# Performance work log

Hardware: AMD Instinct MI355X
Metric: run time of the kernel (lower is better)

## Reference

```python
import jax, jax.numpy as jnp
import numpy as np

HIDDEN = 1024
HEADS = 16
HEAD_DIM = HIDDEN // HEADS
BATCH = 2
SEQ = 2048


def setup_inputs() -> dict:
    key = jax.random.key(0)
    k1, k2, k3 = jax.random.split(key, 3)
    hidden_states = jax.random.normal(k1, (BATCH, SEQ, HIDDEN), dtype=jnp.float32)
    # torch Linear(hidden, 3*hidden) applies x @ W.T; we store the transposed
    # weight directly so the math is x @ W_qkv. Scale ~ fan_in init.
    W_qkv = jax.random.normal(k2, (HIDDEN, 3 * HIDDEN), dtype=jnp.float32) / np.sqrt(HIDDEN)
    W_o = jax.random.normal(k3, (HIDDEN, HIDDEN), dtype=jnp.float32) / np.sqrt(HIDDEN)
    return {"hidden_states": hidden_states, "W_qkv": W_qkv, "W_o": W_o}


def reference(hidden_states, W_qkv, W_o):
    B, S, _ = hidden_states.shape
    scale = 1.0 / np.sqrt(HEAD_DIM)
    qkv = hidden_states @ W_qkv                       # [B, S, 3*H*D]
    qkv = qkv.reshape(B, S, 3, HEADS, HEAD_DIM)
    qkv = jnp.transpose(qkv, (2, 0, 3, 1, 4))         # [3, B, H, S, D]
    q, k, v = qkv[0], qkv[1], qkv[2]
    # The chunked online-softmax path computes exactly softmax(qk^T*scale)v.
    scores = jnp.einsum("bhsd,bhtd->bhst", q, k) * scale  # [B, H, S, S]
    probs = jax.nn.softmax(scores, axis=-1)
    out = jnp.einsum("bhst,bhtd->bhsd", probs, v)     # [B, H, S, D]
    out = jnp.transpose(out, (0, 2, 1, 3)).reshape(B, S, HIDDEN)
    return out @ W_o
```

## Files before the change

kernel.cpp:

```cpp
#include <hip/hip_runtime.h>
#include <hip/hip_bf16.h>
#include <cstdint>

typedef __bf16 bf16_t;
typedef __bf16 bf16x8 __attribute__((ext_vector_type(8)));
typedef __bf16 bf16x4 __attribute__((ext_vector_type(4)));
typedef __bf16 bf16x2 __attribute__((ext_vector_type(2)));
typedef float  f32x4  __attribute__((ext_vector_type(4)));
typedef float  f32x16 __attribute__((ext_vector_type(16)));
typedef unsigned uint4v __attribute__((ext_vector_type(4)));

#define AS1 __attribute__((address_space(1)))
#define AS3 __attribute__((address_space(3)))

static __device__ __forceinline__ void gld_lds16(const void* g, void* l) {
  __builtin_amdgcn_global_load_lds((AS1 void*)g, (AS3 void*)l, 16, 0, 0);
}

static __device__ __forceinline__ unsigned pk2t(float a, float b) {
  return __builtin_amdgcn_perm(__builtin_bit_cast(unsigned, a),
                               __builtin_bit_cast(unsigned, b), 0x03020706u);
}

__global__ __launch_bounds__(256) void prep_k(const float* __restrict__ x,
                                              bf16_t* __restrict__ xb,
                                              const float* __restrict__ wqkv,
                                              bf16_t* __restrict__ wqkvT,
                                              const float* __restrict__ wo,
                                              bf16_t* __restrict__ woT) {
  int bid = blockIdx.x;
  if (bid < 4096) {
    const int i = bid * 256 + threadIdx.x;
    float4 v = ((const float4*)x)[i];
    bf16x4 o;
    o[0] = (bf16_t)v.x; o[1] = (bf16_t)v.y; o[2] = (bf16_t)v.z; o[3] = (bf16_t)v.w;
    *(bf16x4*)(xb + (size_t)i * 4) = o;
    return;
  }
  __shared__ float tile[32][33];
  const float* in; bf16_t* out; int N, bx, by;
  if (bid < 7168) { bid -= 4096; in = wqkv; out = wqkvT; N = 3072; bx = bid % 96; by = bid / 96; }
  else            { bid -= 7168; in = wo;   out = woT;   N = 1024; bx = bid & 31; by = bid >> 5; }
  const int t = threadIdx.x, c = t & 31, r0 = t >> 5;
#pragma unroll
  for (int i = 0; i < 4; ++i) {
    int r = r0 + i * 8;
    tile[r][c] = in[(size_t)(by * 32 + r) * N + bx * 32 + c];
  }
  __syncthreads();
#pragma unroll
  for (int i = 0; i < 4; ++i) {
    int r = r0 + i * 8;
    out[(size_t)(bx * 32 + r) * 1024 + by * 32 + c] = (bf16_t)tile[c][r];
  }
}

template <int KDIM>
static __device__ __forceinline__ void gemm128_pipe(const bf16_t* __restrict__ A,
                                                    const bf16_t* __restrict__ Bt,
                                                    char* lds, f32x4 acc[4][4],
                                                    int bm, int bn) {
  constexpr int NK = KDIM / 32;
  const int t = threadIdx.x;
  const int lr = t & 15, g = (t >> 4) & 3;
  const int w = t >> 6, wr = w >> 1, wc = w & 1;

  auto bufA = [&](int i) { return lds + (i % 3) * 8192; };
  auto bufB = [&](int i) { return lds + 24576 + (i % 3) * 8192; };

  auto stage = [&](int i) {
    const int kt = i * 32;
    char* la = bufA(i);
    char* lb = bufB(i);
#pragma unroll
    for (int c = 0; c < 2; ++c) {
      const int idx = c * 256 + t;
      const int row = idx >> 2, cb = idx & 3;
      const int off = ((t & 192) + c * 256) * 16;
      gld_lds16(A  + (size_t)(bm * 128 + row) * KDIM + kt + cb * 8, la + off);
      gld_lds16(Bt + (size_t)(bn * 128 + row) * KDIM + kt + cb * 8, lb + off);
    }
  };

  stage(0);
  stage(1);
  asm volatile("s_waitcnt vmcnt(4)" ::: "memory");
  __builtin_amdgcn_sched_barrier(0);
  __builtin_amdgcn_s_barrier();

  for (int j = 0; j < NK; ++j) {
    if (j + 2 < NK) {
      stage(j + 2);
      asm volatile("s_waitcnt vmcnt(8)" ::: "memory");
    } else if (j + 1 < NK) {
      asm volatile("s_waitcnt vmcnt(4)" ::: "memory");
    } else {
      asm volatile("s_waitcnt vmcnt(0)" ::: "memory");
    }
    __builtin_amdgcn_sched_barrier(0);
    __builtin_amdgcn_s_barrier();
    const char* laR = bufA(j);
    const char* lbR = bufB(j);
    bf16x8 af[4], bv[4];
#pragma unroll
    for (int mi = 0; mi < 4; ++mi)
      af[mi] = *(const bf16x8*)(laR + (wr * 64 + mi * 16 + lr) * 64 + g * 16);
#pragma unroll
    for (int ni = 0; ni < 4; ++ni)
      bv[ni] = *(const bf16x8*)(lbR + (wc * 64 + ni * 16 + lr) * 64 + g * 16);
    __builtin_amdgcn_s_setprio(1);
#pragma unroll
    for (int mi = 0; mi < 4; ++mi)
#pragma unroll
      for (int ni = 0; ni < 4; ++ni)
        acc[mi][ni] = __builtin_amdgcn_mfma_f32_16x16x32_bf16(af[mi], bv[ni], acc[mi][ni], 0, 0, 0);
    __builtin_amdgcn_s_setprio(0);
    __builtin_amdgcn_sched_barrier(0);
    __builtin_amdgcn_s_barrier();
  }
}

__global__ __launch_bounds__(256) void gemm_qkv_k(const bf16_t* __restrict__ xb,
                                                  const bf16_t* __restrict__ wt,
                                                  bf16_t* __restrict__ Qo,
                                                  bf16_t* __restrict__ Ko,
                                                  bf16_t* __restrict__ Vto) {
  __shared__ __align__(16) char lds[49152];
  const int bm = blockIdx.x, bn = blockIdx.y;
  f32x4 acc[4][4] = {};
  gemm128_pipe<1024>(xb, wt, lds, acc, bm, bn);
  const float cs = 0.18033688011112042f;
  const int t = threadIdx.x, lr = t & 15, g = (t >> 4) & 3, w = t >> 6, wr = w >> 1, wc = w & 1;
  const int row0 = bm * 128 + wr * 64, col0 = bn * 128 + wc * 64;
#pragma unroll
  for (int mi = 0; mi < 4; ++mi) {
    const int row = row0 + mi * 16 + g * 4;
    const int b = row >> 11, s = row & 2047;
#pragma unroll
    for (int ni = 0; ni < 4; ++ni) {
      const int col = col0 + ni * 16 + lr;
      const int t3 = col >> 10, rem = col & 1023, h = rem >> 6, d = rem & 63;
      const int bh = b * 16 + h;
#pragma unroll
      for (int r = 0; r < 4; ++r) {
        const float av = acc[mi][ni][r];
        if (t3 == 0)      Qo[((size_t)bh * 2048 + s + r) * 64 + d] = (bf16_t)(av * cs);
        else if (t3 == 1) Ko[((size_t)bh * 2048 + s + r) * 64 + d] = (bf16_t)av;
        else {
          const int kv = s + r;
          const int q3 = (kv >> 2) & 7;
          const int dq = (q3 & 4) | ((q3 & 1) << 1) | ((q3 >> 1) & 1);
          const int kvp = (kv & ~31) | (dq << 2) | (kv & 3);
          Vto[((size_t)bh * 64 + d) * 2048 + kvp] = (bf16_t)av;
        }
      }
    }
  }
}

__global__ __launch_bounds__(256) void gemm_o_k(const bf16_t* __restrict__ attn,
                                                const bf16_t* __restrict__ wot,
                                                float* __restrict__ out) {
  __shared__ __align__(16) char lds[49152];
  const int bm = blockIdx.x, bn = blockIdx.y;
  f32x4 acc[4][4] = {};
  gemm128_pipe<1024>(attn, wot, lds, acc, bm, bn);
  const int t = threadIdx.x, lr = t & 15, g = (t >> 4) & 3, w = t >> 6, wr = w >> 1, wc = w & 1;
  const int row0 = bm * 128 + wr * 64, col0 = bn * 128 + wc * 64;
#pragma unroll
  for (int mi = 0; mi < 4; ++mi) {
    const int row = row0 + mi * 16 + g * 4;
#pragma unroll
    for (int ni = 0; ni < 4; ++ni) {
      const int col = col0 + ni * 16 + lr;
#pragma unroll
      for (int r = 0; r < 4; ++r)
        out[(size_t)(row + r) * 1024 + col] = acc[mi][ni][r];
    }
  }
}

__global__ __launch_bounds__(256, 2) void attn_k(const bf16_t* __restrict__ Q,
                                                 const bf16_t* __restrict__ K,
                                                 const bf16_t* __restrict__ Vt,
                                                 bf16_t* __restrict__ Ao) {
  __shared__ __align__(16) char smem[32768];
  const int t = threadIdx.x, w = t >> 6, l = t & 63;
  const int ql = l & 31, hi = l >> 5;
  const int orig = blockIdx.y * 16 + blockIdx.x;
  const int swz = (orig & 7) * 64 + (orig >> 3);
  const int qblk = swz & 15, bh = swz >> 4;
  const int b = bh >> 4, h = bh & 15;
  const bf16_t* Qb = Q  + (size_t)bh * 2048 * 64;
  const bf16_t* Kb = K  + (size_t)bh * 2048 * 64;
  const bf16_t* Vb = Vt + (size_t)bh * 64 * 2048;
  const int q0 = qblk * 128 + w * 32;

  const bf16_t* ksrc = Kb + (size_t)l * 64 + w * 8;
  const bf16_t* vsrc = Vb + (size_t)l * 2048 + w * 8;

  char* const kb0 = smem;
  char* const kb1 = smem + 8192;
  char* const vb0 = smem + 16384;
  char* const vb1 = smem + 24576;

  const bf16_t* qp = Qb + (size_t)(q0 + ql) * 64 + hi * 8;
  const bf16x8 qf0 = *(const bf16x8*)(qp);
  const bf16x8 qf1 = *(const bf16x8*)(qp + 16);
  const bf16x8 qf2 = *(const bf16x8*)(qp + 32);
  const bf16x8 qf3 = *(const bf16x8*)(qp + 48);

  bf16x8 ones;
#pragma unroll
  for (int i = 0; i < 8; ++i) ones[i] = (bf16_t)1.0f;

  f32x16 ot0 = {}, ot1 = {}, otls = {};

  auto stageK = [&](int tile, char* dst) {
    const bf16_t* ks = ksrc + (size_t)tile * 4096;
    gld_lds16(ks,      dst + w * 1024);
    gld_lds16(ks + 32, dst + (4 + w) * 1024);
  };
  auto stageV = [&](int tile, char* dst) {
    const bf16_t* vs = vsrc + (size_t)tile * 64;
    gld_lds16(vs,      dst + w * 1024);
    gld_lds16(vs + 32, dst + (4 + w) * 1024);
  };
  auto qk = [&](const char* kbuf, f32x16& sa, f32x16& sb) {
    const bf16x8 ka0 = *(const bf16x8*)(kbuf + (0 + hi) * 1024 + ql * 16);
    const bf16x8 ka1 = *(const bf16x8*)(kbuf + (2 + hi) * 1024 + ql * 16);
    const bf16x8 ka2 = *(const bf16x8*)(kbuf + (4 + hi) * 1024 + ql * 16);
    const bf16x8 ka3 = *(const bf16x8*)(kbuf + (6 + hi) * 1024 + ql * 16);
    sa = __builtin_amdgcn_mfma_f32_32x32x16_bf16(ka0, qf0, sa, 0, 0, 0);
    sa = __builtin_amdgcn_mfma_f32_32x32x16_bf16(ka1, qf1, sa, 0, 0, 0);
    sa = __builtin_amdgcn_mfma_f32_32x32x16_bf16(ka2, qf2, sa, 0, 0, 0);
    sa = __builtin_amdgcn_mfma_f32_32x32x16_bf16(ka3, qf3, sa, 0, 0, 0);
    const bf16x8 kb0f = *(const bf16x8*)(kbuf + (0 + hi) * 1024 + 512 + ql * 16);
    const bf16x8 kb1f = *(const bf16x8*)(kbuf + (2 + hi) * 1024 + 512 + ql * 16);
    const bf16x8 kb2f = *(const bf16x8*)(kbuf + (4 + hi) * 1024 + 512 + ql * 16);
    const bf16x8 kb3f = *(const bf16x8*)(kbuf + (6 + hi) * 1024 + 512 + ql * 16);
    sb = __builtin_amdgcn_mfma_f32_32x32x16_bf16(kb0f, qf0, sb, 0, 0, 0);
    sb = __builtin_amdgcn_mfma_f32_32x32x16_bf16(kb1f, qf1, sb, 0, 0, 0);
    sb = __builtin_amdgcn_mfma_f32_32x32x16_bf16(kb2f, qf2, sb, 0, 0, 0);
    sb = __builtin_amdgcn_mfma_f32_32x32x16_bf16(kb3f, qf3, sb, 0, 0, 0);
  };
  auto sm_pv = [&](const f32x16& sa, const f32x16& sb, const char* vread) {
    uint4v u0 = {pk2t(exp2f(sa[0]),  exp2f(sa[1])),  pk2t(exp2f(sa[2]),  exp2f(sa[3])),
                 pk2t(exp2f(sa[4]),  exp2f(sa[5])),  pk2t(exp2f(sa[6]),  exp2f(sa[7]))};
    uint4v u1 = {pk2t(exp2f(sa[8]),  exp2f(sa[9])),  pk2t(exp2f(sa[10]), exp2f(sa[11])),
                 pk2t(exp2f(sa[12]), exp2f(sa[13])), pk2t(exp2f(sa[14]), exp2f(sa[15]))};
    uint4v u2 = {pk2t(exp2f(sb[0]),  exp2f(sb[1])),  pk2t(exp2f(sb[2]),  exp2f(sb[3])),
                 pk2t(exp2f(sb[4]),  exp2f(sb[5])),  pk2t(exp2f(sb[6]),  exp2f(sb[7]))};
    uint4v u3 = {pk2t(exp2f(sb[8]),  exp2f(sb[9])),  pk2t(exp2f(sb[10]), exp2f(sb[11])),
                 pk2t(exp2f(sb[12]), exp2f(sb[13])), pk2t(exp2f(sb[14]), exp2f(sb[15]))};
    const bf16x8 pf0 = __builtin_bit_cast(bf16x8, u0);
    const bf16x8 pf1 = __builtin_bit_cast(bf16x8, u1);
    const bf16x8 pf2 = __builtin_bit_cast(bf16x8, u2);
    const bf16x8 pf3 = __builtin_bit_cast(bf16x8, u3);
    const bf16x8 v00 = *(const bf16x8*)(vread + (0 + hi) * 1024 + ql * 16);
    const bf16x8 v01 = *(const bf16x8*)(vread + (2 + hi) * 1024 + ql * 16);
    const bf16x8 v02 = *(const bf16x8*)(vread + (4 + hi) * 1024 + ql * 16);
    const bf16x8 v03 = *(const bf16x8*)(vread + (6 + hi) * 1024 + ql * 16);
    const bf16x8 v10 = *(const bf16x8*)(vread + (0 + hi) * 1024 + 512 + ql * 16);
    const bf16x8 v11 = *(const bf16x8*)(vread + (2 + hi) * 1024 + 512 + ql * 16);
    const bf16x8 v12 = *(const bf16x8*)(vread + (4 + hi) * 1024 + 512 + ql * 16);
    const bf16x8 v13 = *(const bf16x8*)(vread + (6 + hi) * 1024 + 512 + ql * 16);
    ot0  = __builtin_amdgcn_mfma_f32_32x32x16_bf16(v00,  pf0, ot0, 0, 0, 0);
    ot1  = __builtin_amdgcn_mfma_f32_32x32x16_bf16(v10,  pf0, ot1, 0, 0, 0);
    otls = __builtin_amdgcn_mfma_f32_32x32x16_bf16(ones, pf0, otls, 0, 0, 0);
    ot0  = __builtin_amdgcn_mfma_f32_32x32x16_bf16(v01,  pf1, ot0, 0, 0, 0);
    ot1  = __builtin_amdgcn_mfma_f32_32x32x16_bf16(v11,  pf1, ot1, 0, 0, 0);
    otls = __builtin_amdgcn_mfma_f32_32x32x16_bf16(ones, pf1, otls, 0, 0, 0);
    ot0  = __builtin_amdgcn_mfma_f32_32x32x16_bf16(v02,  pf2, ot0, 0, 0, 0);
    ot1  = __builtin_amdgcn_mfma_f32_32x32x16_bf16(v12,  pf2, ot1, 0, 0, 0);
    otls = __builtin_amdgcn_mfma_f32_32x32x16_bf16(ones, pf2, otls, 0, 0, 0);
    ot0  = __builtin_amdgcn_mfma_f32_32x32x16_bf16(v03,  pf3, ot0, 0, 0, 0);
    ot1  = __builtin_amdgcn_mfma_f32_32x32x16_bf16(v13,  pf3, ot1, 0, 0, 0);
    otls = __builtin_amdgcn_mfma_f32_32x32x16_bf16(ones, pf3, otls, 0, 0, 0);
  };

  stageK(0, kb0);
  stageV(0, vb0);
  stageK(1, kb1);
  asm volatile("s_waitcnt vmcnt(4)" ::: "memory");
  __builtin_amdgcn_sched_barrier(0);
  __builtin_amdgcn_s_barrier();
  f32x16 sca = {}, scb = {};
  qk(kb0, sca, scb);
  __builtin_amdgcn_s_barrier();

  auto body = [&](int j, char* kstage, const char* kread, const char* vread, char* vstage) {
    if (j < 31) stageV(j + 1, vstage);
    if (j < 30) stageK(j + 2, kstage);
    if (j < 30)      asm volatile("s_waitcnt vmcnt(4)" ::: "memory");
    else if (j == 30) asm volatile("s_waitcnt vmcnt(2)" ::: "memory");
    else             asm volatile("s_waitcnt vmcnt(0)" ::: "memory");
    __builtin_amdgcn_sched_barrier(0);
    __builtin_amdgcn_s_barrier();
    f32x16 sna = {}, snb = {};
    __builtin_amdgcn_s_setprio(1);
    if (j < 31) qk(kread, sna, snb);
    sm_pv(sca, scb, vread);
    __builtin_amdgcn_s_setprio(0);
    __builtin_amdgcn_sched_barrier(0);
    __builtin_amdgcn_s_barrier();
    sca = sna; scb = snb;
  };

#pragma unroll 2
  for (int j = 0; j < 32; ++j) {
    if ((j & 1) == 0) body(j, kb0, kb1, vb0, vb1);
    else              body(j, kb1, kb0, vb1, vb0);
  }

  const float inv = 1.0f / otls[0];
  bf16_t* ob = (bf16_t*)(smem + w * 4096);
#pragma unroll
  for (int rg = 0; rg < 4; ++rg) {
    const int d0 = rg * 8 + hi * 4;
    bf16x4 v0, v1;
#pragma unroll
    for (int j = 0; j < 4; ++j) {
      v0[j] = (bf16_t)(ot0[4 * rg + j] * inv);
      v1[j] = (bf16_t)(ot1[4 * rg + j] * inv);
    }
    *(bf16x4*)((char*)ob + ql * 128 + (((d0)      * 2) ^ ((ql & 7) << 4))) = v0;
    *(bf16x4*)((char*)ob + ql * 128 + (((d0 + 32) * 2) ^ ((ql & 7) << 4))) = v1;
  }
  __syncthreads();
#pragma unroll
  for (int i = 0; i < 4; ++i) {
    const int c = i * 64 + l;
    const int qq = c >> 3, ch = c & 7;
    bf16x8 vv = *(const bf16x8*)((char*)ob + qq * 128 + ((ch * 16) ^ ((qq & 7) << 4)));
    *(bf16x8*)(Ao + (size_t)(b * 2048 + q0 + qq) * 1024 + h * 64 + ch * 8) = vv;
  }
}


extern "C" void kernel_launch(void* const* d_in, const int* in_sizes, int n_in,
                              void* d_out, int out_size, void* d_ws, size_t ws_size,
                              hipStream_t stream) {
  const float* x    = (const float*)d_in[0];
  const float* wqkv = (const float*)d_in[1];
  const float* wo   = (const float*)d_in[2];
  float* out = (float*)d_out;

  char* ws = (char*)d_ws;
  bf16_t* xb    = (bf16_t*)(ws);
  bf16_t* wqkvT = (bf16_t*)(ws + (size_t)(8u  << 20));
  bf16_t* woT   = (bf16_t*)(ws + (size_t)(14u << 20));
  bf16_t* Qb    = (bf16_t*)(ws + (size_t)(16u << 20));
  bf16_t* Kb    = (bf16_t*)(ws + (size_t)(24u << 20));
  bf16_t* Vtb   = (bf16_t*)(ws + (size_t)(32u << 20));
  bf16_t* attn  = (bf16_t*)(ws + (size_t)(40u << 20));

  prep_k<<<8192, 256, 0, stream>>>(x, xb, wqkv, wqkvT, wo, woT);
  gemm_qkv_k<<<dim3(32, 24), 256, 0, stream>>>(xb, wqkvT, Qb, Kb, Vtb);
  attn_k<<<dim3(16, 32), 256, 0, stream>>>(Qb, Kb, Vtb, attn);
  gemm_o_k<<<dim3(32, 8), 256, 0, stream>>>(attn, woT, out);
}
```

Baseline: 119.0 us.

## Swizzle GEMM LDS tiles, shrink output GEMM N-tile, widen input cast

Applies an XOR swizzle to the 16-byte chunk index in the GEMM LDS tiles so that fragment reads spread across banks instead of conflicting. The output projection now uses 128x64 tiles, doubling its grid from 256 to 512 blocks to fill more CUs, at the cost of re-reading more of the A operand. The fp32-to-bf16 input cast also handles 8 elements per thread, halving its block count.

```diff
diff --git a/kernel.cpp b/kernel.cpp
--- a/kernel.cpp
+++ b/kernel.cpp
@@ -29,18 +29,20 @@
                                               const float* __restrict__ wo,
                                               bf16_t* __restrict__ woT) {
   int bid = blockIdx.x;
-  if (bid < 4096) {
+  if (bid < 2048) {
     const int i = bid * 256 + threadIdx.x;
-    float4 v = ((const float4*)x)[i];
-    bf16x4 o;
-    o[0] = (bf16_t)v.x; o[1] = (bf16_t)v.y; o[2] = (bf16_t)v.z; o[3] = (bf16_t)v.w;
-    *(bf16x4*)(xb + (size_t)i * 4) = o;
+    float4 v0 = ((const float4*)x)[(size_t)i * 2];
+    float4 v1 = ((const float4*)x)[(size_t)i * 2 + 1];
+    bf16x8 o;
+    o[0] = (bf16_t)v0.x; o[1] = (bf16_t)v0.y; o[2] = (bf16_t)v0.z; o[3] = (bf16_t)v0.w;
+    o[4] = (bf16_t)v1.x; o[5] = (bf16_t)v1.y; o[6] = (bf16_t)v1.z; o[7] = (bf16_t)v1.w;
+    *(bf16x8*)(xb + (size_t)i * 8) = o;
     return;
   }
   __shared__ float tile[32][33];
   const float* in; bf16_t* out; int N, bx, by;
-  if (bid < 7168) { bid -= 4096; in = wqkv; out = wqkvT; N = 3072; bx = bid % 96; by = bid / 96; }
-  else            { bid -= 7168; in = wo;   out = woT;   N = 1024; bx = bid & 31; by = bid >> 5; }
+  if (bid < 5120) { bid -= 2048; in = wqkv; out = wqkvT; N = 3072; bx = bid % 96; by = bid / 96; }
+  else            { bid -= 5120; in = wo;   out = woT;   N = 1024; bx = bid & 31; by = bid >> 5; }
   const int t = threadIdx.x, c = t & 31, r0 = t >> 5;
 #pragma unroll
   for (int i = 0; i < 4; ++i) {
@@ -64,6 +66,7 @@
   const int t = threadIdx.x;
   const int lr = t & 15, g = (t >> 4) & 3;
   const int w = t >> 6, wr = w >> 1, wc = w & 1;
+  const int xg = (g ^ ((lr >> 1) & 3)) << 4;
 
   auto bufA = [&](int i) { return lds + (i % 3) * 8192; };
   auto bufB = [&](int i) { return lds + 24576 + (i % 3) * 8192; };
@@ -75,7 +78,8 @@
 #pragma unroll
     for (int c = 0; c < 2; ++c) {
       const int idx = c * 256 + t;
-      const int row = idx >> 2, cb = idx & 3;
+      const int row = idx >> 2;
+      const int cb = (idx & 3) ^ ((idx >> 3) & 3);
       const int off = ((t & 192) + c * 256) * 16;
       gld_lds16(A  + (size_t)(bm * 128 + row) * KDIM + kt + cb * 8, la + off);
       gld_lds16(Bt + (size_t)(bn * 128 + row) * KDIM + kt + cb * 8, lb + off);
@@ -104,10 +108,10 @@
     bf16x8 af[4], bv[4];
 #pragma unroll
     for (int mi = 0; mi < 4; ++mi)
-      af[mi] = *(const bf16x8*)(laR + (wr * 64 + mi * 16 + lr) * 64 + g * 16);
+      af[mi] = *(const bf16x8*)(laR + (wr * 64 + mi * 16 + lr) * 64 + xg);
 #pragma unroll
     for (int ni = 0; ni < 4; ++ni)
-      bv[ni] = *(const bf16x8*)(lbR + (wc * 64 + ni * 16 + lr) * 64 + g * 16);
+      bv[ni] = *(const bf16x8*)(lbR + (wc * 64 + ni * 16 + lr) * 64 + xg);
     __builtin_amdgcn_s_setprio(1);
 #pragma unroll
     for (int mi = 0; mi < 4; ++mi)
@@ -158,20 +162,88 @@
   }
 }
 
+static __device__ __forceinline__ void gemm_o_pipe(const bf16_t* __restrict__ A,
+                                                   const bf16_t* __restrict__ Bt,
+                                                   char* lds, f32x4 acc[4][2],
+                                                   int bm, int bn) {
+  constexpr int NK = 32;
+  const int t = threadIdx.x;
+  const int lr = t & 15, g = (t >> 4) & 3;
+  const int w = t >> 6, wr = w >> 1, wc = w & 1;
+  const int xg = (g ^ ((lr >> 1) & 3)) << 4;
+
+  auto bufA = [&](int i) { return lds + (i % 3) * 8192; };
+  auto bufB = [&](int i) { return lds + 24576 + (i % 3) * 4096; };
+
+  auto stage = [&](int i) {
+    const int kt = i * 32;
+    char* la = bufA(i);
+    char* lb = bufB(i);
+#pragma unroll
+    for (int c = 0; c < 2; ++c) {
+      const int idx = c * 256 + t;
+      const int row = idx >> 2;
+      const int cb = (idx & 3) ^ ((idx >> 3) & 3);
+      const int off = ((t & 192) + c * 256) * 16;
+      gld_lds16(A + (size_t)(bm * 128 + row) * 1024 + kt + cb * 8, la + off);
+    }
+    const int rowb = t >> 2;
+    const int cbb = (t & 3) ^ ((t >> 3) & 3);
+    gld_lds16(Bt + (size_t)(bn * 64 + rowb) * 1024 + kt + cbb * 8, lb + (t & 192) * 16);
+  };
+
+  stage(0);
+  stage(1);
+  asm volatile("s_waitcnt vmcnt(3)" ::: "memory");
+  __builtin_amdgcn_sched_barrier(0);
+  __builtin_amdgcn_s_barrier();
+
+  for (int j = 0; j < NK; ++j) {
+    if (j + 2 < NK) {
+      stage(j + 2);
+      asm volatile("s_waitcnt vmcnt(6)" ::: "memory");
+    } else if (j + 1 < NK) {
+      asm volatile("s_waitcnt vmcnt(3)" ::: "memory");
+    } else {
+      asm volatile("s_waitcnt vmcnt(0)" ::: "memory");
+    }
+    __builtin_amdgcn_sched_barrier(0);
+    __builtin_amdgcn_s_barrier();
+    const char* laR = bufA(j);
+    const char* lbR = bufB(j);
+    bf16x8 af[4], bv[2];
+#pragma unroll
+    for (int mi = 0; mi < 4; ++mi)
+      af[mi] = *(const bf16x8*)(laR + (wr * 64 + mi * 16 + lr) * 64 + xg);
+#pragma unroll
+    for (int ni = 0; ni < 2; ++ni)
+      bv[ni] = *(const bf16x8*)(lbR + (wc * 32 + ni * 16 + lr) * 64 + xg);
+    __builtin_amdgcn_s_setprio(1);
+#pragma unroll
+    for (int mi = 0; mi < 4; ++mi)
+#pragma unroll
+      for (int ni = 0; ni < 2; ++ni)
+        acc[mi][ni] = __builtin_amdgcn_mfma_f32_16x16x32_bf16(af[mi], bv[ni], acc[mi][ni], 0, 0, 0);
+    __builtin_amdgcn_s_setprio(0);
+    __builtin_amdgcn_sched_barrier(0);
+    __builtin_amdgcn_s_barrier();
+  }
+}
+
 __global__ __launch_bounds__(256) void gemm_o_k(const bf16_t* __restrict__ attn,
                                                 const bf16_t* __restrict__ wot,
                                                 float* __restrict__ out) {
-  __shared__ __align__(16) char lds[49152];
+  __shared__ __align__(16) char lds[36864];
   const int bm = blockIdx.x, bn = blockIdx.y;
-  f32x4 acc[4][4] = {};
-  gemm128_pipe<1024>(attn, wot, lds, acc, bm, bn);
+  f32x4 acc[4][2] = {};
+  gemm_o_pipe(attn, wot, lds, acc, bm, bn);
   const int t = threadIdx.x, lr = t & 15, g = (t >> 4) & 3, w = t >> 6, wr = w >> 1, wc = w & 1;
-  const int row0 = bm * 128 + wr * 64, col0 = bn * 128 + wc * 64;
+  const int row0 = bm * 128 + wr * 64, col0 = bn * 64 + wc * 32;
 #pragma unroll
   for (int mi = 0; mi < 4; ++mi) {
     const int row = row0 + mi * 16 + g * 4;
 #pragma unroll
-    for (int ni = 0; ni < 4; ++ni) {
+    for (int ni = 0; ni < 2; ++ni) {
       const int col = col0 + ni * 16 + lr;
 #pragma unroll
       for (int r = 0; r < 4; ++r)
@@ -355,8 +427,8 @@
   bf16_t* Vtb   = (bf16_t*)(ws + (size_t)(32u << 20));
   bf16_t* attn  = (bf16_t*)(ws + (size_t)(40u << 20));
 
-  prep_k<<<8192, 256, 0, stream>>>(x, xb, wqkv, wqkvT, wo, woT);
+  prep_k<<<6144, 256, 0, stream>>>(x, xb, wqkv, wqkvT, wo, woT);
   gemm_qkv_k<<<dim3(32, 24), 256, 0, stream>>>(xb, wqkvT, Qb, Kb, Vtb);
   attn_k<<<dim3(16, 32), 256, 0, stream>>>(Qb, Kb, Vtb, attn);
-  gemm_o_k<<<dim3(32, 8), 256, 0, stream>>>(attn, woT, out);
-}
+  gemm_o_k<<<dim3(32, 16), 256, 0, stream>>>(attn, woT, out);
+}
```

Result: no change. 118.1 us (-0.8%).
